# Kernel optimization log

Measured on AMD Instinct MI355X. Metric: run time of the kernel, lower is better.

Reference implementation:

```python
import jax, jax.numpy as jnp
import numpy as np

NUM_LEVELS = 16
LEVEL_DIM = 2
BASE_RES = 16
LOG2_T = 19
TABLE_SIZE = 2 ** LOG2_T
SIZE = 1.0  # default `size` arg of call()

# 8 trilinear corner offsets, shape [8, 3]
OFFSETS = jnp.array([[0, 0, 0], [0, 0, 1], [0, 1, 0], [0, 1, 1],
                     [1, 0, 0], [1, 0, 1], [1, 1, 0], [1, 1, 1]], dtype=jnp.int32)
# Spatial hash primes (uint32 wraparound reproduces TF int64 low-19-bit result exactly)
PRIMES = jnp.array([1, 2654435761, 805459861], dtype=jnp.uint32)


def setup_inputs() -> dict:
    key = jax.random.key(0)
    k1, k2 = jax.random.split(key)
    N = 524288
    x = jax.random.uniform(k1, (N, 3), dtype=jnp.float32)  # in [0,1); call() re-normalizes
    # tf.random_uniform_initializer(minval=-1e-4, maxval=1e-4)
    tables = jax.random.uniform(k2, (NUM_LEVELS, TABLE_SIZE, LEVEL_DIM),
                                dtype=jnp.float32, minval=-1e-4, maxval=1e-4)
    return {"x": x, "tables": tables}


def _encode(x, tables):
    # x: [N, 3] float32, tables: [L, T, D]
    x = jnp.clip((x + SIZE) / (2 * SIZE), 0.0, 1.0 - 1e-6)
    res = (BASE_RES * (2 ** jnp.arange(NUM_LEVELS))).astype(jnp.float32)  # [L]
    scaled = x[None, :, :] * res[:, None, None]          # [L, N, 3]
    floor_f = jnp.floor(scaled)
    frac = scaled - floor_f                              # [L, N, 3]
    floor_i = floor_f.astype(jnp.int32)

    corner = floor_i[:, :, None, :] + OFFSETS[None, None]          # [L, N, 8, 3]
    c = corner.astype(jnp.uint32)
    levels_u = jnp.arange(NUM_LEVELS, dtype=jnp.uint32)[:, None, None]
    hashed = (c[..., 0] * PRIMES[0]) ^ (c[..., 1] * PRIMES[1]) \
             ^ (c[..., 2] * PRIMES[2]) ^ levels_u                  # [L, N, 8]
    idx = (hashed & jnp.uint32(TABLE_SIZE - 1)).astype(jnp.int32)  # mod 2^19

    emb = jax.vmap(lambda t, i: t[i])(tables, idx)                 # [L, N, 8, D]
    # trilinear weights: prod over xyz of frac (if offset==1) else 1-frac
    w = jnp.prod(jnp.where(OFFSETS[None, None] == 1,
                           frac[:, :, None, :], 1.0 - frac[:, :, None, :]),
                 axis=-1)                                          # [L, N, 8]
    out = jnp.sum(emb * w[..., None], axis=2)                      # [L, N, D]
    # concat levels along feature dim -> [N, L*D]
    return out.transpose(1, 0, 2).reshape(x.shape[0], NUM_LEVELS * LEVEL_DIM)


def reference(x, tables):
    return _encode(x, tables)
```

## Files before the change

### kernel.cpp

```cpp
#include <hip/hip_runtime.h>
#include <stdint.h>

#define NUM_LEVELS 16
#define LEVEL_DIM 2
#define BASE_RES 16
#define LOG2_T 19
#define TABLE_SIZE (1u << LOG2_T)
#define TABLE_MASK (TABLE_SIZE - 1u)

#define CPL 256
#define BLOCK 256

typedef float v2f __attribute__((ext_vector_type(2)));
typedef float v4f __attribute__((ext_vector_type(4)));

__device__ __forceinline__ v2f encode_point(
    const float* __restrict__ x, const float* __restrict__ tb,
    int n, float res, uint32_t lv)
{
    float px = __builtin_nontemporal_load(x + (size_t)n * 3 + 0);
    float py = __builtin_nontemporal_load(x + (size_t)n * 3 + 1);
    float pz = __builtin_nontemporal_load(x + (size_t)n * 3 + 2);

    px = fminf(fmaxf((px + 1.0f) * 0.5f, 0.0f), 1.0f - 1e-6f);
    py = fminf(fmaxf((py + 1.0f) * 0.5f, 0.0f), 1.0f - 1e-6f);
    pz = fminf(fmaxf((pz + 1.0f) * 0.5f, 0.0f), 1.0f - 1e-6f);

    float sx = px * res, sy = py * res, sz = pz * res;
    float fx = floorf(sx), fy = floorf(sy), fz = floorf(sz);
    float tx = sx - fx, ty = sy - fy, tz = sz - fz;
    uint32_t ix = (uint32_t)(int32_t)fx;
    uint32_t iy = (uint32_t)(int32_t)fy;
    uint32_t iz = (uint32_t)(int32_t)fz;

    uint32_t hx0 = ix;
    uint32_t hx1 = ix + 1u;
    uint32_t hy0 = iy * 2654435761u;
    uint32_t hy1 = (iy + 1u) * 2654435761u;
    uint32_t hz0 = iz * 805459861u;
    uint32_t hz1 = (iz + 1u) * 805459861u;

    uint32_t idx0 = ((hx0 ^ hy0 ^ hz0 ^ lv) & TABLE_MASK) * 2u;
    uint32_t idx1 = ((hx0 ^ hy0 ^ hz1 ^ lv) & TABLE_MASK) * 2u;
    uint32_t idx2 = ((hx0 ^ hy1 ^ hz0 ^ lv) & TABLE_MASK) * 2u;
    uint32_t idx3 = ((hx0 ^ hy1 ^ hz1 ^ lv) & TABLE_MASK) * 2u;
    uint32_t idx4 = ((hx1 ^ hy0 ^ hz0 ^ lv) & TABLE_MASK) * 2u;
    uint32_t idx5 = ((hx1 ^ hy0 ^ hz1 ^ lv) & TABLE_MASK) * 2u;
    uint32_t idx6 = ((hx1 ^ hy1 ^ hz0 ^ lv) & TABLE_MASK) * 2u;
    uint32_t idx7 = ((hx1 ^ hy1 ^ hz1 ^ lv) & TABLE_MASK) * 2u;

    v2f e0 = *(const v2f*)(tb + idx0);
    v2f e1 = *(const v2f*)(tb + idx1);
    v2f e2 = *(const v2f*)(tb + idx2);
    v2f e3 = *(const v2f*)(tb + idx3);
    v2f e4 = *(const v2f*)(tb + idx4);
    v2f e5 = *(const v2f*)(tb + idx5);
    v2f e6 = *(const v2f*)(tb + idx6);
    v2f e7 = *(const v2f*)(tb + idx7);

    float wx0 = 1.0f - tx, wx1 = tx;
    float wy0 = 1.0f - ty, wy1 = ty;
    float wz0 = 1.0f - tz, wz1 = tz;

    float w0 = wx0 * wy0 * wz0;
    float w1 = wx0 * wy0 * wz1;
    float w2 = wx0 * wy1 * wz0;
    float w3 = wx0 * wy1 * wz1;
    float w4 = wx1 * wy0 * wz0;
    float w5 = wx1 * wy0 * wz1;
    float w6 = wx1 * wy1 * wz0;
    float w7 = wx1 * wy1 * wz1;

    v2f acc;
    acc.x = e0.x * w0 + e1.x * w1 + e2.x * w2 + e3.x * w3
          + e4.x * w4 + e5.x * w5 + e6.x * w6 + e7.x * w7;
    acc.y = e0.y * w0 + e1.y * w1 + e2.y * w2 + e3.y * w3
          + e4.y * w4 + e5.y * w5 + e6.y * w6 + e7.y * w7;
    return acc;
}

__global__ __launch_bounds__(256, 8) void gather_level_kernel(
    const float* __restrict__ x,
    const float* __restrict__ tables,
    float* __restrict__ ws,
    int N)
{
    int g = blockIdx.x;
    int half  = g / (8 * CPL);
    int h     = g % (8 * CPL);
    int level = (h & 7) + 8 * half;
    int chunk = h >> 3;
    int P     = (N + CPL - 1) / CPL;
    int base  = chunk * P;

    const float* tb = tables + (size_t)level * TABLE_SIZE * LEVEL_DIM;
    v2f* wrow = (v2f*)ws + (size_t)level * N;
    float res = (float)(BASE_RES << level);
    uint32_t lv = (uint32_t)level;

    for (int i = threadIdx.x; i < P; i += 2 * BLOCK) {
        int n0 = base + i;
        int n1 = base + i + BLOCK;
        bool ok0 = (n0 < N);
        bool ok1 = (i + BLOCK < P) && (n1 < N);

        if (ok0 && ok1) {
            v2f a0 = encode_point(x, tb, n0, res, lv);
            v2f a1 = encode_point(x, tb, n1, res, lv);
            __builtin_nontemporal_store(a0, wrow + n0);
            __builtin_nontemporal_store(a1, wrow + n1);
        } else if (ok0) {
            v2f a0 = encode_point(x, tb, n0, res, lv);
            __builtin_nontemporal_store(a0, wrow + n0);
        }
    }
}

__global__ __launch_bounds__(256) void transpose_kernel(
    const float* __restrict__ ws, float* __restrict__ out, int N)
{
    int n = blockIdx.x * blockDim.x + threadIdx.x;
    if (n >= N) return;

    v2f v[NUM_LEVELS];
    #pragma unroll
    for (int l = 0; l < NUM_LEVELS; ++l)
        v[l] = __builtin_nontemporal_load((const v2f*)ws + (size_t)l * N + n);

    v4f* o = (v4f*)(out + (size_t)n * (NUM_LEVELS * LEVEL_DIM));
    #pragma unroll
    for (int i = 0; i < 8; ++i) {
        v4f t;
        t.x = v[2 * i].x;     t.y = v[2 * i].y;
        t.z = v[2 * i + 1].x; t.w = v[2 * i + 1].y;
        o[i] = t;
    }
}

__global__ __launch_bounds__(256) void hashenc_fallback(
    const float* __restrict__ x, const float* __restrict__ tables,
    float* __restrict__ out, int N)
{
    int n = blockIdx.x * blockDim.x + threadIdx.x;
    if (n >= N) return;
    float* op = out + (size_t)n * (NUM_LEVELS * LEVEL_DIM);
    #pragma unroll 4
    for (int l = 0; l < NUM_LEVELS; ++l) {
        const float* tb = tables + (size_t)l * TABLE_SIZE * LEVEL_DIM;
        v2f a = encode_point(x, tb, n, (float)(BASE_RES << l), (uint32_t)l);
        *(v2f*)(op + l * 2) = a;
    }
}

extern "C" void kernel_launch(void* const* d_in, const int* in_sizes, int n_in,
                              void* d_out, int out_size, void* d_ws, size_t ws_size,
                              hipStream_t stream) {
    const float* x      = (const float*)d_in[0];
    const float* tables = (const float*)d_in[1];
    float* out          = (float*)d_out;
    int N = in_sizes[0] / 3;

    size_t ws_needed = (size_t)NUM_LEVELS * N * LEVEL_DIM * sizeof(float);
    if (ws_size >= ws_needed) {
        float* ws = (float*)d_ws;
        gather_level_kernel<<<NUM_LEVELS * CPL, BLOCK, 0, stream>>>(x, tables, ws, N);
        transpose_kernel<<<(N + BLOCK - 1) / BLOCK, BLOCK, 0, stream>>>(ws, out, N);
    } else {
        hashenc_fallback<<<(N + BLOCK - 1) / BLOCK, BLOCK, 0, stream>>>(x, tables, out, N);
    }
}
```

Measured before the change: 433.9 us.

## Sweep all levels per point in gather kernel instead of one level per block

Replaces the per-level block assignment, where each block handled one level for a chunk of points, with a kernel where each thread loads a point once and loops over all 16 levels, writing each level's result to the workspace. This removes 16x redundant loads and normalisation of x. It gives up the per-level grouping of blocks, which kept each level's 4 MB table hot in cache (8 levels at a time within each half of the grid). Scattered accesses now span all 16 tables at once, so L2/MALL hit rates may drop. The fallback kernel is also changed to normalise x once.

```diff
diff --git a/kernel.cpp b/kernel.cpp
--- a/kernel.cpp
+++ b/kernel.cpp
@@ -8,24 +8,16 @@
 #define TABLE_SIZE (1u << LOG2_T)
 #define TABLE_MASK (TABLE_SIZE - 1u)
 
-#define CPL 256
 #define BLOCK 256
+#define GBLOCKS 2048
 
 typedef float v2f __attribute__((ext_vector_type(2)));
 typedef float v4f __attribute__((ext_vector_type(4)));
 
-__device__ __forceinline__ v2f encode_point(
-    const float* __restrict__ x, const float* __restrict__ tb,
-    int n, float res, uint32_t lv)
+__device__ __forceinline__ v2f encode_level(
+    const float* __restrict__ tb,
+    float px, float py, float pz, float res, uint32_t lv)
 {
-    float px = __builtin_nontemporal_load(x + (size_t)n * 3 + 0);
-    float py = __builtin_nontemporal_load(x + (size_t)n * 3 + 1);
-    float pz = __builtin_nontemporal_load(x + (size_t)n * 3 + 2);
-
-    px = fminf(fmaxf((px + 1.0f) * 0.5f, 0.0f), 1.0f - 1e-6f);
-    py = fminf(fmaxf((py + 1.0f) * 0.5f, 0.0f), 1.0f - 1e-6f);
-    pz = fminf(fmaxf((pz + 1.0f) * 0.5f, 0.0f), 1.0f - 1e-6f);
-
     float sx = px * res, sy = py * res, sz = pz * res;
     float fx = floorf(sx), fy = floorf(sy), fz = floorf(sz);
     float tx = sx - fx, ty = sy - fy, tz = sz - fz;
@@ -79,39 +71,32 @@
     return acc;
 }
 
-__global__ __launch_bounds__(256, 8) void gather_level_kernel(
+__global__ __launch_bounds__(256, 8) void gather_sweep_kernel(
     const float* __restrict__ x,
     const float* __restrict__ tables,
     float* __restrict__ ws,
     int N)
 {
-    int g = blockIdx.x;
-    int half  = g / (8 * CPL);
-    int h     = g % (8 * CPL);
-    int level = (h & 7) + 8 * half;
-    int chunk = h >> 3;
-    int P     = (N + CPL - 1) / CPL;
-    int base  = chunk * P;
+    int P = (N + GBLOCKS - 1) / GBLOCKS;
+    int base = blockIdx.x * P;
 
-    const float* tb = tables + (size_t)level * TABLE_SIZE * LEVEL_DIM;
-    v2f* wrow = (v2f*)ws + (size_t)level * N;
-    float res = (float)(BASE_RES << level);
-    uint32_t lv = (uint32_t)level;
+    for (int i = threadIdx.x; i < P; i += BLOCK) {
+        int n = base + i;
+        if (n >= N) break;
 
-    for (int i = threadIdx.x; i < P; i += 2 * BLOCK) {
-        int n0 = base + i;
-        int n1 = base + i + BLOCK;
-        bool ok0 = (n0 < N);
-        bool ok1 = (i + BLOCK < P) && (n1 < N);
+        float px = __builtin_nontemporal_load(x + (size_t)n * 3 + 0);
+        float py = __builtin_nontemporal_load(x + (size_t)n * 3 + 1);
+        float pz = __builtin_nontemporal_load(x + (size_t)n * 3 + 2);
+        px = fminf(fmaxf((px + 1.0f) * 0.5f, 0.0f), 1.0f - 1e-6f);
+        py = fminf(fmaxf((py + 1.0f) * 0.5f, 0.0f), 1.0f - 1e-6f);
+        pz = fminf(fmaxf((pz + 1.0f) * 0.5f, 0.0f), 1.0f - 1e-6f);
 
-        if (ok0 && ok1) {
-            v2f a0 = encode_point(x, tb, n0, res, lv);
-            v2f a1 = encode_point(x, tb, n1, res, lv);
-            __builtin_nontemporal_store(a0, wrow + n0);
-            __builtin_nontemporal_store(a1, wrow + n1);
-        } else if (ok0) {
-            v2f a0 = encode_point(x, tb, n0, res, lv);
-            __builtin_nontemporal_store(a0, wrow + n0);
+        #pragma unroll 2
+        for (int l = 0; l < NUM_LEVELS; ++l) {
+            const float* tb = tables + (size_t)l * TABLE_SIZE * LEVEL_DIM;
+            v2f acc = encode_level(tb, px, py, pz,
+                                   (float)(BASE_RES << l), (uint32_t)l);
+            __builtin_nontemporal_store(acc, (v2f*)ws + (size_t)l * N + n);
         }
     }
 }
@@ -143,11 +128,17 @@
 {
     int n = blockIdx.x * blockDim.x + threadIdx.x;
     if (n >= N) return;
+    float px = x[(size_t)n * 3 + 0];
+    float py = x[(size_t)n * 3 + 1];
+    float pz = x[(size_t)n * 3 + 2];
+    px = fminf(fmaxf((px + 1.0f) * 0.5f, 0.0f), 1.0f - 1e-6f);
+    py = fminf(fmaxf((py + 1.0f) * 0.5f, 0.0f), 1.0f - 1e-6f);
+    pz = fminf(fmaxf((pz + 1.0f) * 0.5f, 0.0f), 1.0f - 1e-6f);
     float* op = out + (size_t)n * (NUM_LEVELS * LEVEL_DIM);
     #pragma unroll 4
     for (int l = 0; l < NUM_LEVELS; ++l) {
         const float* tb = tables + (size_t)l * TABLE_SIZE * LEVEL_DIM;
-        v2f a = encode_point(x, tb, n, (float)(BASE_RES << l), (uint32_t)l);
+        v2f a = encode_level(tb, px, py, pz, (float)(BASE_RES << l), (uint32_t)l);
         *(v2f*)(op + l * 2) = a;
     }
 }
@@ -163,7 +154,7 @@
     size_t ws_needed = (size_t)NUM_LEVELS * N * LEVEL_DIM * sizeof(float);
     if (ws_size >= ws_needed) {
         float* ws = (float*)d_ws;
-        gather_level_kernel<<<NUM_LEVELS * CPL, BLOCK, 0, stream>>>(x, tables, ws, N);
+        gather_sweep_kernel<<<GBLOCKS, BLOCK, 0, stream>>>(x, tables, ws, N);
         transpose_kernel<<<(N + BLOCK - 1) / BLOCK, BLOCK, 0, stream>>>(ws, out, N);
     } else {
         hashenc_fallback<<<(N + BLOCK - 1) / BLOCK, BLOCK, 0, stream>>>(x, tables, out, N);
```

Measured after the change: 552.1 us. +27.2%, slower.
